# Kernel tuning notes

Hardware: AMD Instinct MI355X
Metric: run time of the kernel (lower is better)

Reference implementation:

```python
import jax, jax.numpy as jnp
import numpy as np

N_HEAD = 8
DIM_K = 64
DIM_MODEL = N_HEAD * DIM_K  # 512; must equal seq_len for the final batch_dot
SCALE = DIM_K ** 0.5


def setup_inputs() -> dict:
    key = jax.random.key(0)
    ks = jax.random.split(key, 4)
    B, S, D_IN = 32, 512, 128
    x = jax.random.normal(ks[0], (B, S, D_IN), dtype=jnp.float32)
    init = 0.02
    Wq = jax.random.normal(ks[1], (D_IN * N_HEAD, DIM_MODEL), dtype=jnp.float32) * init
    Wk = jax.random.normal(ks[2], (D_IN * N_HEAD, DIM_MODEL), dtype=jnp.float32) * init
    Wv = jax.random.normal(ks[3], (D_IN * N_HEAD, DIM_MODEL), dtype=jnp.float32) * init
    z = jnp.zeros((DIM_MODEL,), dtype=jnp.float32)
    return {"x": x, "Wq": Wq, "bq": z, "Wk": Wk, "bk": z, "Wv": Wv, "bv": z}


def reference(x, Wq, bq, Wk, bk, Wv, bv):
    # Tile input n_head times along feature dim (matches K.concatenate([q]*n_head))
    xt = jnp.concatenate([x] * N_HEAD, axis=-1)          # [B, S, d_in*n_head]
    q = xt @ Wq + bq                                      # [B, S, dim_model]
    k = xt @ Wk + bk
    v = xt @ Wv + bv
    # K.batch_dot(q, k, axes=[-1,-1]) -> q @ k^T per batch
    scores = jnp.einsum('bsd,btd->bst', q, k) / SCALE     # [B, S, S]
    attn = jax.nn.softmax(scores, axis=-1)
    # K.batch_dot(v, attn, axes=[2,-1]): out[b,i,j] = sum_k v[b,i,k]*attn[b,j,k]
    # (only valid because S == dim_model, as in the original buggy layer)
    out = jnp.einsum('bik,bjk->bij', v, attn)             # [B, S, S]
    return out
```

## Files before the change

kernel.cpp:

```cpp
#include <hip/hip_runtime.h>


typedef unsigned short u16;
typedef __attribute__((ext_vector_type(8))) short bf16x8;
typedef __attribute__((ext_vector_type(4))) float f32x4;
typedef __attribute__((ext_vector_type(2))) float f32x2;
typedef __attribute__((ext_vector_type(2))) unsigned int u32x2;

__device__ inline u16 f2bf(float f) {
  unsigned u = __float_as_uint(f);
  u = u + 0x7fffu + ((u >> 16) & 1u);
  return (u16)(u >> 16);
}
__device__ inline float bf2f(u16 h) { return __uint_as_float(((unsigned)h) << 16); }

__device__ inline void gl16(const u16* g, u16* l) {
  __builtin_amdgcn_global_load_lds(
      (const __attribute__((address_space(1))) unsigned int*)g,
      (__attribute__((address_space(3))) unsigned int*)l, 16, 0, 0);
}

#define VM0  asm volatile("s_waitcnt vmcnt(0)" ::: "memory")
#define LK0  asm volatile("s_waitcnt lgkmcnt(0)" ::: "memory")
#define SB0  __builtin_amdgcn_sched_barrier(0)

__global__ __launch_bounds__(256)
void prep_all(const float* __restrict__ x,
              const float* __restrict__ Wq, const float* __restrict__ Wk,
              const float* __restrict__ Wv,
              u16* __restrict__ WTh, u16* __restrict__ WTl,
              u16* __restrict__ xh, u16* __restrict__ xl) {
  if (blockIdx.x < 96) {
    __shared__ float sm[128][17];
    int t  = blockIdx.x >> 5;
    int nb = blockIdx.x & 31;
    const float* W = (t == 0) ? Wq : (t == 1) ? Wk : Wv;
    int n0 = nb << 4;
    int nl = threadIdx.x & 15;
    int kq = threadIdx.x >> 4;
    float s[8];
#pragma unroll
    for (int i = 0; i < 8; ++i) s[i] = 0.f;
#pragma unroll
    for (int h = 0; h < 8; ++h)
#pragma unroll
      for (int i = 0; i < 8; ++i)
        s[i] += W[(h * 128 + kq + (i << 4)) * 512 + n0 + nl];
#pragma unroll
    for (int i = 0; i < 8; ++i) sm[kq + (i << 4)][nl] = s[i];
    __syncthreads();
    int no = threadIdx.x >> 4;
    int k8 = (threadIdx.x & 15) << 3;
    bf16x8 h8, l8;
#pragma unroll
    for (int c = 0; c < 8; ++c) {
      float v = sm[k8 + c][no];
      u16 h = f2bf(v);
      h8[c] = (short)h;
      l8[c] = (short)f2bf(v - bf2f(h));
    }
    long o = (long)t * 65536 + (long)(n0 + no) * 128 + k8;
    *(bf16x8*)&WTh[o] = h8;
    *(bf16x8*)&WTl[o] = l8;
  } else {
    int i = (blockIdx.x - 96) * 256 + threadIdx.x;
    const f32x4* xx = (const f32x4*)x;
    f32x4 a = xx[i * 2], b = xx[i * 2 + 1];
    float v[8] = {a[0], a[1], a[2], a[3], b[0], b[1], b[2], b[3]};
    bf16x8 h8, l8;
#pragma unroll
    for (int j = 0; j < 8; ++j) {
      u16 h = f2bf(v[j]);
      h8[j] = (short)h;
      l8[j] = (short)f2bf(v[j] - bf2f(h));
    }
    ((bf16x8*)xh)[i] = h8;
    ((bf16x8*)xl)[i] = l8;
  }
}

__global__ __launch_bounds__(256, 2)
void proj_fused(const u16* __restrict__ xh, const u16* __restrict__ xl,
                const u16* __restrict__ WTh, const u16* __restrict__ WTl,
                u16* __restrict__ Qh, u16* __restrict__ Kh, u16* __restrict__ Vh,
                const float* __restrict__ bq, const float* __restrict__ bk,
                const float* __restrict__ bv) {
  __shared__ __align__(16) char ldsraw[65536];
  u16* st = (u16*)ldsraw;

  int tid = threadIdx.x;
  int bid = blockIdx.x;
  bid = (bid & 7) * 192 + (bid >> 3);
  int which = bid % 3;
  int tile  = bid / 3;
  int mt = tile >> 2;
  int nt = tile & 3;

  const u16* Ah = xh + (long)mt * (128 * 128);
  const u16* Al = xl + (long)mt * (128 * 128);
  const u16* Bh = WTh + which * 65536 + nt * 16384;
  const u16* Bl = WTl + which * 65536 + nt * 16384;
  const float* bias = (which == 0) ? bq : (which == 1) ? bk : bv;
  u16* C = (which == 0) ? Qh : (which == 1) ? Kh : Vh;

  int lane = tid & 63;
  int wv = tid >> 6;
  int wm = (wv >> 1) << 6;
  int wn = (wv & 1) << 6;
  int frow = lane & 15;
  int fk = (lane >> 4) << 3;

  f32x4 acc[4][4];
#pragma unroll
  for (int i = 0; i < 4; ++i)
#pragma unroll
    for (int j = 0; j < 4; ++j) {
      f32x4 z = {0.f, 0.f, 0.f, 0.f};
      acc[i][j] = z;
    }

  for (int kk = 0; kk < 2; ++kk) {
    int k0 = kk << 6;
#pragma unroll
    for (int j = 0; j < 4; ++j) {
      int c = j * 256 + tid;
      int row = c >> 3;
      int scol = ((c & 7) ^ (row & 7)) << 3;
      int ga = row * 128 + k0 + scol;
      int lo = c << 3;
      gl16(Ah + ga, st + lo);
      gl16(Al + ga, st + 8192 + lo);
      gl16(Bh + ga, st + 16384 + lo);
      gl16(Bl + ga, st + 24576 + lo);
    }
    __syncthreads();
#pragma unroll
    for (int ks = 0; ks < 2; ++ks) {
      int kb = (ks << 5) + fk;
      bf16x8 a_h[4], a_l[4], b_h[4], b_l[4];
#pragma unroll
      for (int i = 0; i < 4; ++i) {
        int ar = wm + (i << 4) + frow;
        int ao = ar * 64 + (kb ^ ((ar & 7) << 3));
        a_h[i] = *(const bf16x8*)&st[ao];
        a_l[i] = *(const bf16x8*)&st[8192 + ao];
        int br = wn + (i << 4) + frow;
        int bo = br * 64 + (kb ^ ((br & 7) << 3));
        b_h[i] = *(const bf16x8*)&st[16384 + bo];
        b_l[i] = *(const bf16x8*)&st[24576 + bo];
      }
#pragma unroll
      for (int i = 0; i < 4; ++i)
#pragma unroll
        for (int j = 0; j < 4; ++j) {
          acc[i][j] = __builtin_amdgcn_mfma_f32_16x16x32_bf16(a_h[i], b_h[j], acc[i][j], 0, 0, 0);
          acc[i][j] = __builtin_amdgcn_mfma_f32_16x16x32_bf16(a_l[i], b_h[j], acc[i][j], 0, 0, 0);
          acc[i][j] = __builtin_amdgcn_mfma_f32_16x16x32_bf16(a_h[i], b_l[j], acc[i][j], 0, 0, 0);
        }
    }
    __syncthreads();
  }

  float* tr = ((float*)ldsraw) + wv * 2112;
  int lr = lane >> 3;
  int c8 = (lane & 7) << 3;
  int colbase = (nt << 7) + wn + c8;
  float bb[8];
#pragma unroll
  for (int c = 0; c < 8; ++c) bb[c] = bias[colbase + c];
  long rowg0 = (long)(mt << 7) + wm;
#pragma unroll
  for (int q = 0; q < 2; ++q) {
#pragma unroll
    for (int il = 0; il < 2; ++il) {
      int i = (q << 1) + il;
#pragma unroll
      for (int j = 0; j < 4; ++j)
#pragma unroll
        for (int r = 0; r < 4; ++r)
          tr[((il << 4) + ((lane >> 4) << 2) + r) * 66 + (j << 4) + (lane & 15)] =
              acc[i][j][r];
    }
#pragma unroll
    for (int p = 0; p < 4; ++p) {
      int rr = (p << 3) + lr;
      float v[8];
      *(f32x2*)&v[0] = *(const f32x2*)&tr[rr * 66 + c8];
      *(f32x2*)&v[2] = *(const f32x2*)&tr[rr * 66 + c8 + 2];
      *(f32x2*)&v[4] = *(const f32x2*)&tr[rr * 66 + c8 + 4];
      *(f32x2*)&v[6] = *(const f32x2*)&tr[rr * 66 + c8 + 6];
      bf16x8 o8;
#pragma unroll
      for (int c = 0; c < 8; ++c) o8[c] = (short)f2bf(v[c] + bb[c]);
      *(bf16x8*)&C[(rowg0 + (q << 5) + rr) * 512 + colbase] = o8;
    }
  }
}

__global__ __launch_bounds__(512, 4)
void attn_fused(const u16* __restrict__ Q, const u16* __restrict__ K,
                const u16* __restrict__ V, float* __restrict__ OUT) {
  __shared__ __align__(16) char LDS[67584];
  u16* QP = (u16*)LDS;
  u16* B  = (u16*)(LDS + 32768);
  float* smax = (float*)(LDS + 65536);
  float* ssum = (float*)(LDS + 66560);

  int tid = threadIdx.x;
  int p = blockIdx.x;
  int xcd = p & 7, idx = p >> 3;
  int b  = (xcd << 2) + (idx >> 4);
  int jb = idx & 15;

  const u16* Qp = Q + ((long)b * 512 + jb * 32) * 512;
  const u16* Kp = K + (long)b * 262144;
  const u16* Vp = V + (long)b * 262144;

  int lane = tid & 63, nw = tid >> 6;
  int frow = lane & 15, hi4 = lane >> 4;
  u16* myB = B + (nw << 11);
  int tokbase = nw << 6;

  auto stageW = [&](const u16* src, int k0) {
#pragma unroll
    for (int j = 0; j < 4; ++j) {
      int u = (j << 6) + lane;
      int tok = u >> 2, slot = u & 3;
      gl16(src + (long)(tokbase + tok) * 512 + k0 + ((slot ^ ((tok >> 1) & 3)) << 3),
           myB + (u << 3));
    }
  };
  auto rW = [&](int r) -> bf16x8 {
    return *(const bf16x8*)&myB[(r << 5) + ((hi4 ^ ((r >> 1) & 3)) << 3)];
  };
  auto rQ = [&](int row, int sl) -> bf16x8 {
    return *(const bf16x8*)&QP[(row << 9) + ((sl ^ (row & 7)) << 3)];
  };
  auto rP = [&](int row, int sl) -> bf16x8 {
    return *(const bf16x8*)(LDS + (((row << 10) + (sl << 4)) ^ ((row & 7) << 4)));
  };

#pragma unroll
  for (int j = 0; j < 4; ++j) {
    int u = (j << 9) + tid;
    int row = u >> 6, sl = u & 63;
    gl16(Qp + (long)row * 512 + ((sl ^ (row & 7)) << 3), QP + (u << 3));
  }
  stageW(Kp, 0);
  __syncthreads();

  f32x4 acc[4][2];
#pragma unroll
  for (int jj = 0; jj < 4; ++jj)
#pragma unroll
    for (int ii = 0; ii < 2; ++ii) {
      f32x4 z = {0.f, 0.f, 0.f, 0.f};
      acc[jj][ii] = z;
    }

  for (int s = 0; s < 16; ++s) {
    if (s) VM0;
    bf16x8 qf[2], af[4];
#pragma unroll
    for (int ii = 0; ii < 2; ++ii)
      qf[ii] = rQ((ii << 4) + frow, (s << 2) + hi4);
#pragma unroll
    for (int jj = 0; jj < 4; ++jj)
      af[jj] = rW((jj << 4) + frow);
    LK0; SB0;
    if (s < 15) stageW(Kp, (s + 1) << 5);
    else        stageW(Vp, 0);
    __builtin_amdgcn_s_setprio(1);
#pragma unroll
    for (int jj = 0; jj < 4; ++jj)
#pragma unroll
      for (int ii = 0; ii < 2; ++ii)
        acc[jj][ii] = __builtin_amdgcn_mfma_f32_16x16x32_bf16(
            af[jj], qf[ii], acc[jj][ii], 0, 0, 0);
    __builtin_amdgcn_s_setprio(0);
  }

  float mx[2], sm[2], inv_[2];
#pragma unroll
  for (int ii = 0; ii < 2; ++ii) {
    float m = acc[0][ii][0];
#pragma unroll
    for (int jj = 0; jj < 4; ++jj)
#pragma unroll
      for (int r = 0; r < 4; ++r) m = fmaxf(m, acc[jj][ii][r]);
    m = fmaxf(m, __shfl_xor(m, 16));
    m = fmaxf(m, __shfl_xor(m, 32));
    mx[ii] = m;
  }
  if (hi4 == 0) {
#pragma unroll
    for (int ii = 0; ii < 2; ++ii) smax[(((ii << 4) + frow) << 3) + nw] = mx[ii];
  }
  __syncthreads();
#pragma unroll
  for (int ii = 0; ii < 2; ++ii) {
    f32x4 a = *(const f32x4*)&smax[((ii << 4) + frow) << 3];
    f32x4 c = *(const f32x4*)&smax[((((ii << 4) + frow) << 3) + 4)];
    mx[ii] = fmaxf(fmaxf(fmaxf(a[0], a[1]), fmaxf(a[2], a[3])),
                   fmaxf(fmaxf(c[0], c[1]), fmaxf(c[2], c[3])));
    sm[ii] = 0.f;
  }
#pragma unroll
  for (int jj = 0; jj < 4; ++jj)
#pragma unroll
    for (int ii = 0; ii < 2; ++ii)
#pragma unroll
      for (int r = 0; r < 4; ++r) {
        float pv = __expf((acc[jj][ii][r] - mx[ii]) * 0.125f);
        acc[jj][ii][r] = pv;
        sm[ii] += pv;
      }
#pragma unroll
  for (int ii = 0; ii < 2; ++ii) {
    sm[ii] += __shfl_xor(sm[ii], 16);
    sm[ii] += __shfl_xor(sm[ii], 32);
  }
  if (hi4 == 0) {
#pragma unroll
    for (int ii = 0; ii < 2; ++ii) ssum[(((ii << 4) + frow) << 3) + nw] = sm[ii];
  }
  __syncthreads();
#pragma unroll
  for (int ii = 0; ii < 2; ++ii) {
    f32x4 a = *(const f32x4*)&ssum[((ii << 4) + frow) << 3];
    f32x4 c = *(const f32x4*)&ssum[((((ii << 4) + frow) << 3) + 4)];
    inv_[ii] = 1.f / (a[0] + a[1] + a[2] + a[3] + c[0] + c[1] + c[2] + c[3]);
  }
#pragma unroll
  for (int ii = 0; ii < 2; ++ii) {
    int qr = (ii << 4) + frow;
    int rowoff = qr << 10;
    int swz = (qr & 7) << 4;
#pragma unroll
    for (int jj = 0; jj < 4; ++jj) {
      int c0 = ((nw << 6) + (jj << 4) + (hi4 << 2)) << 1;
      unsigned lo = (unsigned)f2bf(acc[jj][ii][0] * inv_[ii]) |
                    ((unsigned)f2bf(acc[jj][ii][1] * inv_[ii]) << 16);
      unsigned hi = (unsigned)f2bf(acc[jj][ii][2] * inv_[ii]) |
                    ((unsigned)f2bf(acc[jj][ii][3] * inv_[ii]) << 16);
      u32x2 w = {lo, hi};
      *(u32x2*)(LDS + ((rowoff + c0) ^ swz)) = w;
    }
  }
  __syncthreads();

  f32x4 o[4][2];
#pragma unroll
  for (int jj = 0; jj < 4; ++jj)
#pragma unroll
    for (int ii = 0; ii < 2; ++ii) {
      f32x4 z = {0.f, 0.f, 0.f, 0.f};
      o[jj][ii] = z;
    }

  for (int s = 0; s < 16; ++s) {
    if (s) VM0;
    bf16x8 pf[2], vf[4];
#pragma unroll
    for (int ii = 0; ii < 2; ++ii)
      pf[ii] = rP((ii << 4) + frow, (s << 2) + hi4);
#pragma unroll
    for (int jj = 0; jj < 4; ++jj)
      vf[jj] = rW((jj << 4) + frow);
    LK0; SB0;
    if (s < 15) stageW(Vp, (s + 1) << 5);
    __builtin_amdgcn_s_setprio(1);
#pragma unroll
    for (int jj = 0; jj < 4; ++jj)
#pragma unroll
      for (int ii = 0; ii < 2; ++ii)
        o[jj][ii] = __builtin_amdgcn_mfma_f32_16x16x32_bf16(
            vf[jj], pf[ii], o[jj][ii], 0, 0, 0);
    __builtin_amdgcn_s_setprio(0);
  }

  float* Ob = OUT + (long)b * 262144 + jb * 32;
#pragma unroll
  for (int jj = 0; jj < 4; ++jj)
#pragma unroll
    for (int ii = 0; ii < 2; ++ii)
#pragma unroll
      for (int r = 0; r < 4; ++r) {
        int vrow = (nw << 6) + (jj << 4) + (hi4 << 2) + r;
        int qc = (ii << 4) + frow;
        Ob[(long)vrow * 512 + qc] = o[jj][ii][r];
      }
}

extern "C" void kernel_launch(void* const* d_in, const int* in_sizes, int n_in,
                              void* d_out, int out_size, void* d_ws, size_t ws_size,
                              hipStream_t stream) {
  const float* x  = (const float*)d_in[0];
  const float* Wq = (const float*)d_in[1];
  const float* bq = (const float*)d_in[2];
  const float* Wk = (const float*)d_in[3];
  const float* bk = (const float*)d_in[4];
  const float* Wv = (const float*)d_in[5];
  const float* bv = (const float*)d_in[6];
  float* out = (float*)d_out;

  char* ws = (char*)d_ws;
  size_t off = 0;
  auto alloc = [&](size_t bytes) -> char* {
    char* p = ws + off;
    off = (off + bytes + 255) & ~(size_t)255;
    return p;
  };
  u16* WTh = (u16*)alloc((size_t)3 * 512 * 128 * 2);
  u16* WTl = (u16*)alloc((size_t)3 * 512 * 128 * 2);
  u16* xh  = (u16*)alloc((size_t)16384 * 128 * 2);
  u16* xl  = (u16*)alloc((size_t)16384 * 128 * 2);
  u16* Qh  = (u16*)alloc((size_t)16384 * 512 * 2);
  u16* Kh  = (u16*)alloc((size_t)16384 * 512 * 2);
  u16* Vh  = (u16*)alloc((size_t)16384 * 512 * 2);

  prep_all<<<1120, 256, 0, stream>>>(x, Wq, Wk, Wv, WTh, WTl, xh, xl);
  proj_fused<<<1536, 256, 0, stream>>>(xh, xl, WTh, WTl, Qh, Kh, Vh, bq, bk, bv);
  attn_fused<<<512, 512, 0, stream>>>(Qh, Kh, Vh, out);
}
```

Measured before the change: 91.29 us.

## Double attention query tile to 64 rows and switch to 32x32x16 MFMA

Each attention block now handles 64 query rows instead of 32, which halves the grid and halves how often K and V are re-streamed per batch. The inner products move from 16x16x32 to 32x32x16 MFMA tiles, with a new LDS swizzle and fragment mapping to match. LDS per block grows to about 100KB and the occupancy hint drops from 4 to 2 blocks. With only 256 blocks for 256 CUs, latency hiding may be weaker.

```diff
diff --git a/kernel.cpp b/kernel.cpp
--- a/kernel.cpp
+++ b/kernel.cpp
@@ -3,6 +3,7 @@
 
 typedef unsigned short u16;
 typedef __attribute__((ext_vector_type(8))) short bf16x8;
+typedef __attribute__((ext_vector_type(16))) float f32x16;
 typedef __attribute__((ext_vector_type(4))) float f32x4;
 typedef __attribute__((ext_vector_type(2))) float f32x2;
 typedef __attribute__((ext_vector_type(2))) unsigned int u32x2;
@@ -197,27 +198,27 @@
   }
 }
 
-__global__ __launch_bounds__(512, 4)
+__global__ __launch_bounds__(512, 2)
 void attn_fused(const u16* __restrict__ Q, const u16* __restrict__ K,
                 const u16* __restrict__ V, float* __restrict__ OUT) {
-  __shared__ __align__(16) char LDS[67584];
+  __shared__ __align__(16) char LDS[102400];
   u16* QP = (u16*)LDS;
-  u16* B  = (u16*)(LDS + 32768);
-  float* smax = (float*)(LDS + 65536);
-  float* ssum = (float*)(LDS + 66560);
+  u16* B  = (u16*)(LDS + 65536);
+  float* smax = (float*)(LDS + 98304);
+  float* ssum = (float*)(LDS + 100352);
 
   int tid = threadIdx.x;
   int p = blockIdx.x;
   int xcd = p & 7, idx = p >> 3;
-  int b  = (xcd << 2) + (idx >> 4);
-  int jb = idx & 15;
-
-  const u16* Qp = Q + ((long)b * 512 + jb * 32) * 512;
+  int b  = (xcd << 2) + (idx >> 3);
+  int jb = idx & 7;
+
+  const u16* Qp = Q + ((long)b * 512 + jb * 64) * 512;
   const u16* Kp = K + (long)b * 262144;
   const u16* Vp = V + (long)b * 262144;
 
   int lane = tid & 63, nw = tid >> 6;
-  int frow = lane & 15, hi4 = lane >> 4;
+  int l31 = lane & 31, l5 = lane >> 5;
   u16* myB = B + (nw << 11);
   int tokbase = nw << 6;
 
@@ -225,23 +226,23 @@
 #pragma unroll
     for (int j = 0; j < 4; ++j) {
       int u = (j << 6) + lane;
-      int tok = u >> 2, slot = u & 3;
-      gl16(src + (long)(tokbase + tok) * 512 + k0 + ((slot ^ ((tok >> 1) & 3)) << 3),
-           myB + (u << 3));
+      int tok = u >> 2, sl = u & 3;
+      int ps = (sl ^ (tok & 3) ^ ((tok >> 2) & 3)) & 3;
+      gl16(src + (long)(tokbase + tok) * 512 + k0 + (ps << 3), myB + (u << 3));
     }
   };
-  auto rW = [&](int r) -> bf16x8 {
-    return *(const bf16x8*)&myB[(r << 5) + ((hi4 ^ ((r >> 1) & 3)) << 3)];
+  auto rA = [&](int c, int ks) -> bf16x8 {
+    int tok = (c << 5) + l31;
+    int sl = (ks << 1) + l5;
+    int ps = (sl ^ (tok & 3) ^ ((tok >> 2) & 3)) & 3;
+    return *(const bf16x8*)&myB[(tok << 5) + (ps << 3)];
   };
-  auto rQ = [&](int row, int sl) -> bf16x8 {
-    return *(const bf16x8*)&QP[(row << 9) + ((sl ^ (row & 7)) << 3)];
+  auto rQ = [&](int q, int sl) -> bf16x8 {
+    return *(const bf16x8*)&QP[(q << 9) + ((sl ^ (q & 7)) << 3)];
   };
-  auto rP = [&](int row, int sl) -> bf16x8 {
-    return *(const bf16x8*)(LDS + (((row << 10) + (sl << 4)) ^ ((row & 7) << 4)));
-  };
-
-#pragma unroll
-  for (int j = 0; j < 4; ++j) {
+
+#pragma unroll
+  for (int j = 0; j < 8; ++j) {
     int u = (j << 9) + tid;
     int row = u >> 6, sl = u & 63;
     gl16(Qp + (long)row * 512 + ((sl ^ (row & 7)) << 3), QP + (u << 3));
@@ -249,146 +250,148 @@
   stageW(Kp, 0);
   __syncthreads();
 
-  f32x4 acc[4][2];
-#pragma unroll
-  for (int jj = 0; jj < 4; ++jj)
-#pragma unroll
-    for (int ii = 0; ii < 2; ++ii) {
-      f32x4 z = {0.f, 0.f, 0.f, 0.f};
-      acc[jj][ii] = z;
-    }
+  f32x16 acc[2][2];
+#pragma unroll
+  for (int c = 0; c < 2; ++c)
+#pragma unroll
+    for (int j = 0; j < 2; ++j)
+#pragma unroll
+      for (int r = 0; r < 16; ++r) acc[c][j][r] = 0.f;
 
   for (int s = 0; s < 16; ++s) {
     if (s) VM0;
-    bf16x8 qf[2], af[4];
-#pragma unroll
-    for (int ii = 0; ii < 2; ++ii)
-      qf[ii] = rQ((ii << 4) + frow, (s << 2) + hi4);
-#pragma unroll
-    for (int jj = 0; jj < 4; ++jj)
-      af[jj] = rW((jj << 4) + frow);
+    bf16x8 af[2][2], qf[2][2];
+#pragma unroll
+    for (int ks = 0; ks < 2; ++ks) {
+#pragma unroll
+      for (int c = 0; c < 2; ++c) af[ks][c] = rA(c, ks);
+#pragma unroll
+      for (int j = 0; j < 2; ++j)
+        qf[ks][j] = rQ((j << 5) + l31, (s << 2) + (ks << 1) + l5);
+    }
     LK0; SB0;
     if (s < 15) stageW(Kp, (s + 1) << 5);
     else        stageW(Vp, 0);
     __builtin_amdgcn_s_setprio(1);
 #pragma unroll
-    for (int jj = 0; jj < 4; ++jj)
-#pragma unroll
-      for (int ii = 0; ii < 2; ++ii)
-        acc[jj][ii] = __builtin_amdgcn_mfma_f32_16x16x32_bf16(
-            af[jj], qf[ii], acc[jj][ii], 0, 0, 0);
+    for (int ks = 0; ks < 2; ++ks)
+#pragma unroll
+      for (int c = 0; c < 2; ++c)
+#pragma unroll
+        for (int j = 0; j < 2; ++j)
+          acc[c][j] = __builtin_amdgcn_mfma_f32_32x32x16_bf16(
+              af[ks][c], qf[ks][j], acc[c][j], 0, 0, 0);
     __builtin_amdgcn_s_setprio(0);
   }
 
   float mx[2], sm[2], inv_[2];
 #pragma unroll
-  for (int ii = 0; ii < 2; ++ii) {
-    float m = acc[0][ii][0];
-#pragma unroll
-    for (int jj = 0; jj < 4; ++jj)
-#pragma unroll
-      for (int r = 0; r < 4; ++r) m = fmaxf(m, acc[jj][ii][r]);
-    m = fmaxf(m, __shfl_xor(m, 16));
+  for (int j = 0; j < 2; ++j) {
+    float m = acc[0][j][0];
+#pragma unroll
+    for (int c = 0; c < 2; ++c)
+#pragma unroll
+      for (int r = 0; r < 16; ++r) m = fmaxf(m, acc[c][j][r]);
     m = fmaxf(m, __shfl_xor(m, 32));
-    mx[ii] = m;
-  }
-  if (hi4 == 0) {
-#pragma unroll
-    for (int ii = 0; ii < 2; ++ii) smax[(((ii << 4) + frow) << 3) + nw] = mx[ii];
+    mx[j] = m;
+  }
+  if (l5 == 0) {
+#pragma unroll
+    for (int j = 0; j < 2; ++j) smax[(((j << 5) + l31) << 3) + nw] = mx[j];
   }
   __syncthreads();
 #pragma unroll
-  for (int ii = 0; ii < 2; ++ii) {
-    f32x4 a = *(const f32x4*)&smax[((ii << 4) + frow) << 3];
-    f32x4 c = *(const f32x4*)&smax[((((ii << 4) + frow) << 3) + 4)];
-    mx[ii] = fmaxf(fmaxf(fmaxf(a[0], a[1]), fmaxf(a[2], a[3])),
-                   fmaxf(fmaxf(c[0], c[1]), fmaxf(c[2], c[3])));
-    sm[ii] = 0.f;
-  }
-#pragma unroll
-  for (int jj = 0; jj < 4; ++jj)
-#pragma unroll
-    for (int ii = 0; ii < 2; ++ii)
-#pragma unroll
-      for (int r = 0; r < 4; ++r) {
-        float pv = __expf((acc[jj][ii][r] - mx[ii]) * 0.125f);
-        acc[jj][ii][r] = pv;
-        sm[ii] += pv;
+  for (int j = 0; j < 2; ++j) {
+    f32x4 a = *(const f32x4*)&smax[((j << 5) + l31) << 3];
+    f32x4 c = *(const f32x4*)&smax[((((j << 5) + l31) << 3) + 4)];
+    mx[j] = fmaxf(fmaxf(fmaxf(a[0], a[1]), fmaxf(a[2], a[3])),
+                  fmaxf(fmaxf(c[0], c[1]), fmaxf(c[2], c[3])));
+    sm[j] = 0.f;
+  }
+#pragma unroll
+  for (int c = 0; c < 2; ++c)
+#pragma unroll
+    for (int j = 0; j < 2; ++j)
+#pragma unroll
+      for (int r = 0; r < 16; ++r) {
+        float pv = __expf((acc[c][j][r] - mx[j]) * 0.125f);
+        acc[c][j][r] = pv;
+        sm[j] += pv;
       }
 #pragma unroll
-  for (int ii = 0; ii < 2; ++ii) {
-    sm[ii] += __shfl_xor(sm[ii], 16);
-    sm[ii] += __shfl_xor(sm[ii], 32);
-  }
-  if (hi4 == 0) {
-#pragma unroll
-    for (int ii = 0; ii < 2; ++ii) ssum[(((ii << 4) + frow) << 3) + nw] = sm[ii];
+  for (int j = 0; j < 2; ++j) sm[j] += __shfl_xor(sm[j], 32);
+  if (l5 == 0) {
+#pragma unroll
+    for (int j = 0; j < 2; ++j) ssum[(((j << 5) + l31) << 3) + nw] = sm[j];
   }
   __syncthreads();
 #pragma unroll
-  for (int ii = 0; ii < 2; ++ii) {
-    f32x4 a = *(const f32x4*)&ssum[((ii << 4) + frow) << 3];
-    f32x4 c = *(const f32x4*)&ssum[((((ii << 4) + frow) << 3) + 4)];
-    inv_[ii] = 1.f / (a[0] + a[1] + a[2] + a[3] + c[0] + c[1] + c[2] + c[3]);
-  }
-#pragma unroll
-  for (int ii = 0; ii < 2; ++ii) {
-    int qr = (ii << 4) + frow;
-    int rowoff = qr << 10;
-    int swz = (qr & 7) << 4;
-#pragma unroll
-    for (int jj = 0; jj < 4; ++jj) {
-      int c0 = ((nw << 6) + (jj << 4) + (hi4 << 2)) << 1;
-      unsigned lo = (unsigned)f2bf(acc[jj][ii][0] * inv_[ii]) |
-                    ((unsigned)f2bf(acc[jj][ii][1] * inv_[ii]) << 16);
-      unsigned hi = (unsigned)f2bf(acc[jj][ii][2] * inv_[ii]) |
-                    ((unsigned)f2bf(acc[jj][ii][3] * inv_[ii]) << 16);
-      u32x2 w = {lo, hi};
-      *(u32x2*)(LDS + ((rowoff + c0) ^ swz)) = w;
-    }
+  for (int j = 0; j < 2; ++j) {
+    f32x4 a = *(const f32x4*)&ssum[((j << 5) + l31) << 3];
+    f32x4 c = *(const f32x4*)&ssum[((((j << 5) + l31) << 3) + 4)];
+    inv_[j] = 1.f / (a[0] + a[1] + a[2] + a[3] + c[0] + c[1] + c[2] + c[3]);
+  }
+#pragma unroll
+  for (int j = 0; j < 2; ++j) {
+    int q = (j << 5) + l31;
+    int rowoff = q << 10;
+    int swz = (q & 7) << 4;
+#pragma unroll
+    for (int c = 0; c < 2; ++c)
+#pragma unroll
+      for (int g = 0; g < 4; ++g) {
+        int col = (nw << 6) + (c << 5) + (g << 3) + (l5 << 2);
+        unsigned lo = (unsigned)f2bf(acc[c][j][(g << 2) + 0] * inv_[j]) |
+                      ((unsigned)f2bf(acc[c][j][(g << 2) + 1] * inv_[j]) << 16);
+        unsigned hi = (unsigned)f2bf(acc[c][j][(g << 2) + 2] * inv_[j]) |
+                      ((unsigned)f2bf(acc[c][j][(g << 2) + 3] * inv_[j]) << 16);
+        u32x2 w = {lo, hi};
+        *(u32x2*)(LDS + ((rowoff + (col << 1)) ^ swz)) = w;
+      }
   }
   __syncthreads();
 
-  f32x4 o[4][2];
-#pragma unroll
-  for (int jj = 0; jj < 4; ++jj)
-#pragma unroll
-    for (int ii = 0; ii < 2; ++ii) {
-      f32x4 z = {0.f, 0.f, 0.f, 0.f};
-      o[jj][ii] = z;
-    }
+#pragma unroll
+  for (int c = 0; c < 2; ++c)
+#pragma unroll
+    for (int j = 0; j < 2; ++j)
+#pragma unroll
+      for (int r = 0; r < 16; ++r) acc[c][j][r] = 0.f;
 
   for (int s = 0; s < 16; ++s) {
     if (s) VM0;
-    bf16x8 pf[2], vf[4];
-#pragma unroll
-    for (int ii = 0; ii < 2; ++ii)
-      pf[ii] = rP((ii << 4) + frow, (s << 2) + hi4);
-#pragma unroll
-    for (int jj = 0; jj < 4; ++jj)
-      vf[jj] = rW((jj << 4) + frow);
+    bf16x8 vf[2][2], pf[2][2];
+#pragma unroll
+    for (int ks = 0; ks < 2; ++ks) {
+#pragma unroll
+      for (int c = 0; c < 2; ++c) vf[ks][c] = rA(c, ks);
+#pragma unroll
+      for (int j = 0; j < 2; ++j)
+        pf[ks][j] = rQ((j << 5) + l31, (s << 2) + (ks << 1) + l5);
+    }
     LK0; SB0;
     if (s < 15) stageW(Vp, (s + 1) << 5);
     __builtin_amdgcn_s_setprio(1);
 #pragma unroll
-    for (int jj = 0; jj < 4; ++jj)
-#pragma unroll
-      for (int ii = 0; ii < 2; ++ii)
-        o[jj][ii] = __builtin_amdgcn_mfma_f32_16x16x32_bf16(
-            vf[jj], pf[ii], o[jj][ii], 0, 0, 0);
+    for (int ks = 0; ks < 2; ++ks)
+#pragma unroll
+      for (int c = 0; c < 2; ++c)
+#pragma unroll
+        for (int j = 0; j < 2; ++j)
+          acc[c][j] = __builtin_amdgcn_mfma_f32_32x32x16_bf16(
+              vf[ks][c], pf[ks][j], acc[c][j], 0, 0, 0);
     __builtin_amdgcn_s_setprio(0);
   }
 
-  float* Ob = OUT + (long)b * 262144 + jb * 32;
-#pragma unroll
-  for (int jj = 0; jj < 4; ++jj)
-#pragma unroll
-    for (int ii = 0; ii < 2; ++ii)
-#pragma unroll
-      for (int r = 0; r < 4; ++r) {
-        int vrow = (nw << 6) + (jj << 4) + (hi4 << 2) + r;
-        int qc = (ii << 4) + frow;
-        Ob[(long)vrow * 512 + qc] = o[jj][ii][r];
+  float* Ob = OUT + (long)b * 262144 + jb * 64;
+#pragma unroll
+  for (int c = 0; c < 2; ++c)
+#pragma unroll
+    for (int j = 0; j < 2; ++j)
+#pragma unroll
+      for (int r = 0; r < 16; ++r) {
+        int vtok = (nw << 6) + (c << 5) + (r & 3) + ((r >> 2) << 3) + (l5 << 2);
+        Ob[(long)vtok * 512 + (j << 5) + l31] = acc[c][j][r];
       }
 }
 
@@ -421,5 +424,5 @@
 
   prep_all<<<1120, 256, 0, stream>>>(x, Wq, Wk, Wv, WTh, WTl, xh, xl);
   proj_fused<<<1536, 256, 0, stream>>>(xh, xl, WTh, WTl, Qh, Kh, Vh, bq, bk, bv);
-  attn_fused<<<512, 512, 0, stream>>>(Qh, Kh, Vh, out);
-}
+  attn_fused<<<256, 512, 0, stream>>>(Qh, Kh, Vh, out);
+}
```

New measurement: 82.94 us. 1.1x faster.
